# Optimization experiments

Hardware: AMD Instinct MI355X
Metric: run time of the kernel (lower is better)

## Reference

```python
import jax, jax.numpy as jnp
import numpy as np

TAU_MIN, TAU_MAX = 5.0, 50.0
BOOST = 3.2
DECO_RATE = 0.01

B, I, F, Q = 4096, 1024, 2048, 4

def setup_inputs() -> dict:
    key = jax.random.key(0)
    ks = jax.random.split(key, 12)
    return {
        "inputs": jax.random.normal(ks[0], (B, I), jnp.float32),
        "hidden_state": jax.random.normal(ks[1], (B, F), jnp.float32),
        "W_in": jax.random.normal(ks[2], (I, F), jnp.float32) / np.sqrt(I),
        "b_in": jnp.zeros((F,), jnp.float32),
        "amp_real": jax.random.normal(ks[3], (F, Q), jnp.float32) * 0.1,
        "amp_imag": jax.random.normal(ks[4], (F, Q), jnp.float32) * 0.1,
        "phase": jax.random.uniform(ks[5], (F, Q), jnp.float32, 0.0, 2 * np.pi),
        "primary": jax.random.normal(ks[6], (F, F), jnp.float32) / np.sqrt(F),
        "ent_mat": jax.random.normal(ks[7], (F, F), jnp.float32) / np.sqrt(F),
        "corr": jax.random.uniform(ks[8], (F,), jnp.float32, 0.0, 0.7),
        "W_tau": jax.random.uniform(ks[9], (F, F), jnp.float32, 0.0, 0.1) / np.sqrt(F),
        "b_tau": jnp.zeros((F,), jnp.float32),
        "W_dec": jax.random.uniform(ks[10], (F, F), jnp.float32, 0.0, 0.5) / np.sqrt(F),
        "b_dec": jnp.zeros((F,), jnp.float32),
        "time_step": 1,
    }

def reference(inputs, hidden_state, W_in, b_in, amp_real, amp_imag, phase,
              primary, ent_mat, corr, W_tau, b_tau, W_dec, b_dec, time_step):
    t = jnp.float32(time_step)
    batch = inputs.shape[0]
    feats = hidden_state.shape[1]

    # input projection: [B,I] @ [I,F]
    x_proj = inputs @ W_in + b_in

    # quantum superposition state (batch-independent, [F,Q] params)
    ph = phase + t * 0.1
    real_c = amp_real * jnp.cos(ph)          # [F,Q]
    imag_c = amp_imag * jnp.sin(ph)          # [F,Q]
    sup_r = real_c.sum(-1)                    # [F]
    sup_i = imag_c.sum(-1)                    # [F]
    prob_amp = real_c ** 2 + imag_c ** 2      # [F,Q]
    q_state = sup_r * jnp.exp(-sup_i ** 2)    # [F]
    q_state_b = jnp.broadcast_to(q_state, (batch, feats))
    prob_amp_b = jnp.broadcast_to(prob_amp, (batch,) + prob_amp.shape)

    # entangled recurrent connections: two F x F matmuls
    ent_rec = hidden_state @ primary + (hidden_state @ ent_mat) * corr

    # quantum time constants
    tau_raw = q_state_b @ W_tau + b_tau
    tau_q = (TAU_MIN + (TAU_MAX - TAU_MIN) * jax.nn.sigmoid(tau_raw)) / BOOST

    # decoherence gate
    deco = jax.nn.sigmoid(q_state_b @ W_dec + b_dec)
    coherent = jnp.exp(-DECO_RATE * t)

    classical = jnp.tanh(x_proj + ent_rec)
    quantum_act = q_state_b * deco * coherent
    combined = classical + quantum_act

    dx_dt = (-hidden_state + combined) / tau_q
    dt_q = 0.1 / BOOST
    new_hidden = hidden_state + dt_q * dx_dt

    # diagnostics
    d_amp = jnp.mean(prob_amp_b, axis=-1)          # [B,F]
    d_coh = coherent
    d_ent = jnp.mean(jnp.abs(ent_rec))
    d_dec = jnp.mean(deco)
    d_tau = jnp.mean(tau_q)
    return (new_hidden, d_amp, d_coh, d_ent, d_dec, d_tau)
```

## Files before the change

kernel.cpp:

```cpp
#include <hip/hip_runtime.h>
#include <hip/hip_bf16.h>

#define BD 4096
#define ID 1024
#define FD 2048

typedef __bf16 v8bf __attribute__((ext_vector_type(8)));
typedef float  v4f  __attribute__((ext_vector_type(4)));

struct alignas(8) bf4 { __hip_bfloat16 x, y, z, w; };

__device__ inline __hip_bfloat16 bf(float f) { return __float2bfloat16(f); }
__device__ inline float sig(float x) { return 1.f / (1.f + expf(-x)); }

__device__ inline void gload16(const __hip_bfloat16* g, __hip_bfloat16* l) {
  __builtin_amdgcn_global_load_lds(
      (const __attribute__((address_space(1))) void*)g,
      (__attribute__((address_space(3))) void*)l, 16, 0, 0);
}

__global__ void k_prep_q(const float* ar, const float* ai, const float* ph,
                         const int* tstep, float* qs, float* pamp,
                         float* scal, float* tau_raw, float* dec_raw) {
  int j = blockIdx.x * 256 + threadIdx.x;
  if (j < 4) scal[j] = 0.f;
  if (j < FD) { tau_raw[j] = 0.f; dec_raw[j] = 0.f; }
  if (j >= FD) return;
  float t = (float)tstep[0];
  float4 a = ((const float4*)ar)[j];
  float4 b = ((const float4*)ai)[j];
  float4 p = ((const float4*)ph)[j];
  float sr = 0.f, si = 0.f, pm = 0.f;
  {
    float c, s, rc, ic;
    c = cosf(p.x + 0.1f * t); s = sinf(p.x + 0.1f * t);
    rc = a.x * c; ic = b.x * s; sr += rc; si += ic; pm += rc * rc + ic * ic;
    c = cosf(p.y + 0.1f * t); s = sinf(p.y + 0.1f * t);
    rc = a.y * c; ic = b.y * s; sr += rc; si += ic; pm += rc * rc + ic * ic;
    c = cosf(p.z + 0.1f * t); s = sinf(p.z + 0.1f * t);
    rc = a.z * c; ic = b.z * s; sr += rc; si += ic; pm += rc * rc + ic * ic;
    c = cosf(p.w + 0.1f * t); s = sinf(p.w + 0.1f * t);
    rc = a.w * c; ic = b.w * s; sr += rc; si += ic; pm += rc * rc + ic * ic;
  }
  qs[j] = sr * expf(-si * si);
  pamp[j] = 0.25f * pm;
}

__global__ void k_cast(const float* s1, __hip_bfloat16* d1, int n1,
                       const float* s2, __hip_bfloat16* d2) {
  int i = blockIdx.x * blockDim.x + threadIdx.x;
  const float* src = s1; __hip_bfloat16* dst = d1;
  if (i >= n1) { i -= n1; src = s2; dst = d2; }
  float4 v = ((const float4*)src)[i];
  bf4 o{bf(v.x), bf(v.y), bf(v.z), bf(v.w)};
  ((bf4*)dst)[i] = o;
}

__global__ void k_tcast(const float* src, const float* src2, const float* corr,
                        __hip_bfloat16* dst, int R, int C, int useM) {
  __shared__ float t[32][33];
  int tx = threadIdx.x, ty = threadIdx.y;
  int x = blockIdx.x * 32 + tx;
  int yb = blockIdx.y * 32;
  float cr = useM ? corr[x] : 0.f;
#pragma unroll
  for (int j = 0; j < 4; j++) {
    int y = yb + ty + j * 8;
    float v = src[(size_t)y * C + x];
    if (useM) v += src2[(size_t)y * C + x] * cr;
    t[ty + j * 8][tx] = v;
  }
  __syncthreads();
#pragma unroll
  for (int j = 0; j < 4; j++) {
    int orow = blockIdx.x * 32 + ty + j * 8;
    int ocol = yb + tx;
    dst[(size_t)orow * R + ocol] = bf(t[tx][ty + j * 8]);
  }
}

__global__ void k_matvec(const float* qs, const float* Wt, const float* Wd,
                         float* tau_raw, float* dec_raw) {
  int j = blockIdx.x * 256 + threadIdx.x;
  int i0 = blockIdx.y * 128;
  const float* W = blockIdx.z ? Wd : Wt;
  float* out = blockIdx.z ? dec_raw : tau_raw;
  __shared__ float q[128];
  if (threadIdx.x < 128) q[threadIdx.x] = qs[i0 + threadIdx.x];
  __syncthreads();
  float acc = 0.f;
#pragma unroll 8
  for (int i = 0; i < 128; i++) acc = fmaf(q[i], W[(size_t)(i0 + i) * FD + j], acc);
  atomicAdd(&out[j], acc);
}

__global__ void k_post(const float* tau_raw, const float* dec_raw, const float* qs,
                       const float* b_tau, const float* b_dec, const int* tstep,
                       float* s_arr, float* qact, float* scal) {
  int j = blockIdx.x * 256 + threadIdx.x;
  float t = (float)tstep[0];
  float coh = expf(-0.01f * t);
  float tq = (5.f + 45.f * sig(tau_raw[j] + b_tau[j])) / 3.2f;
  s_arr[j] = 0.03125f / tq;
  float dec = sig(dec_raw[j] + b_dec[j]);
  qact[j] = qs[j] * dec * coh;
  float tsum = tq, dsum = dec;
  for (int off = 32; off; off >>= 1) {
    tsum += __shfl_down(tsum, off);
    dsum += __shfl_down(dsum, off);
  }
  __shared__ float rt[4], rd[4];
  int w = threadIdx.x >> 6;
  if ((threadIdx.x & 63) == 0) { rt[w] = tsum; rd[w] = dsum; }
  __syncthreads();
  if (threadIdx.x == 0) {
    atomicAdd(&scal[1], rd[0] + rd[1] + rd[2] + rd[3]);
    atomicAdd(&scal[2], rt[0] + rt[1] + rt[2] + rt[3]);
  }
}

__global__ __launch_bounds__(256, 4) void k_gemm(
    const __hip_bfloat16* __restrict__ Ah,
    const __hip_bfloat16* __restrict__ MT,
    const __hip_bfloat16* __restrict__ Ax,
    const __hip_bfloat16* __restrict__ WT,
    const float* __restrict__ b_in, const float* __restrict__ s_arr,
    const float* __restrict__ qact,
    float* ent_sum, float* __restrict__ out) {
  __shared__ alignas(16) __hip_bfloat16 As[2][128][32];
  __shared__ alignas(16) __hip_bfloat16 Bs[2][64][32];
  __shared__ float red[4];

  const int tid = threadIdx.x;
  const int l = tid & 63, w = tid >> 6;
  const int wr = w >> 1, wc = w & 1;
  const int row0 = blockIdx.x * 128, col0 = blockIdx.y * 64;

  v4f acc[4][2];
#pragma unroll
  for (int i = 0; i < 4; i++)
#pragma unroll
    for (int j = 0; j < 2; j++) acc[i][j] = (v4f)0.f;

  auto stage = [&](int buf, const __hip_bfloat16* A, int lda,
                   const __hip_bfloat16* B, int ldb, int k) {
    gload16(A + (size_t)(row0 + w * 32 + (l >> 2)) * lda + k + (l & 3) * 8,
            &As[buf][w * 32][0]);
    gload16(A + (size_t)(row0 + w * 32 + 16 + (l >> 2)) * lda + k + (l & 3) * 8,
            &As[buf][w * 32 + 16][0]);
    gload16(B + (size_t)(col0 + w * 16 + (l >> 2)) * ldb + k + (l & 3) * 8,
            &Bs[buf][w * 16][0]);
  };
  auto compute = [&](int buf) {
    v8bf a[4], b[2];
#pragma unroll
    for (int mi = 0; mi < 4; mi++)
      a[mi] = *(const v8bf*)&As[buf][wr * 64 + mi * 16 + (l & 15)][(l >> 4) * 8];
#pragma unroll
    for (int ni = 0; ni < 2; ni++)
      b[ni] = *(const v8bf*)&Bs[buf][wc * 32 + ni * 16 + (l & 15)][(l >> 4) * 8];
#pragma unroll
    for (int mi = 0; mi < 4; mi++)
#pragma unroll
      for (int ni = 0; ni < 2; ni++)
        acc[mi][ni] = __builtin_amdgcn_mfma_f32_16x16x32_bf16(a[mi], b[ni], acc[mi][ni], 0, 0, 0);
  };

  stage(0, Ah, FD, MT, FD, 0);
  __syncthreads();
  for (int kt = 0; kt < FD / 32; kt++) {
    if (kt + 1 < FD / 32) stage((kt + 1) & 1, Ah, FD, MT, FD, (kt + 1) * 32);
    compute(kt & 1);
    __syncthreads();
  }

  float asum = 0.f;
#pragma unroll
  for (int mi = 0; mi < 4; mi++)
#pragma unroll
    for (int ni = 0; ni < 2; ni++)
#pragma unroll
      for (int e = 0; e < 4; e++) asum += fabsf(acc[mi][ni][e]);

  stage(0, Ax, ID, WT, ID, 0);
  __syncthreads();
  for (int kt = 0; kt < ID / 32; kt++) {
    if (kt + 1 < ID / 32) stage((kt + 1) & 1, Ax, ID, WT, ID, (kt + 1) * 32);
    compute(kt & 1);
    __syncthreads();
  }

  for (int off = 32; off; off >>= 1) asum += __shfl_down(asum, off);
  if (l == 0) red[w] = asum;
  __syncthreads();
  if (tid == 0) atomicAdd(ent_sum, red[0] + red[1] + red[2] + red[3]);

#pragma unroll
  for (int ni = 0; ni < 2; ni++) {
    int gc = col0 + wc * 32 + ni * 16 + (l & 15);
    float bi = b_in[gc], qa = qact[gc], sj = s_arr[gc];
#pragma unroll
    for (int mi = 0; mi < 4; mi++) {
      int gr0 = row0 + wr * 64 + mi * 16 + (l >> 4) * 4;
#pragma unroll
      for (int e = 0; e < 4; e++) {
        int gr = gr0 + e;
        float comb = tanhf(acc[mi][ni][e] + bi) + qa;
        float h = __bfloat162float(Ah[(size_t)gr * FD + gc]);
        out[(size_t)gr * FD + gc] = fmaf(sj, comb - h, h);
      }
    }
  }
}

__global__ void k_damp(const float* __restrict__ pamp, const float* scal,
                       const int* tstep, float* __restrict__ out1, float* out3) {
  int i = blockIdx.x * 256 + threadIdx.x;
  int c = (i * 4) & (FD - 1);
  ((float4*)out1)[i] = *(const float4*)&pamp[c];
  if (i == 0) {
    float t = (float)tstep[0];
    out3[0] = expf(-0.01f * t);
    out3[1] = scal[0] / (float)((size_t)BD * FD);
    out3[2] = scal[1] / (float)FD;
    out3[3] = scal[2] / (float)FD;
  }
}

extern "C" void kernel_launch(void* const* d_in, const int* in_sizes, int n_in,
                              void* d_out, int out_size, void* d_ws, size_t ws_size,
                              hipStream_t stream) {
  const float* inputs  = (const float*)d_in[0];
  const float* hidden  = (const float*)d_in[1];
  const float* W_in    = (const float*)d_in[2];
  const float* b_in    = (const float*)d_in[3];
  const float* amp_r   = (const float*)d_in[4];
  const float* amp_i   = (const float*)d_in[5];
  const float* phase   = (const float*)d_in[6];
  const float* primary = (const float*)d_in[7];
  const float* ent_mat = (const float*)d_in[8];
  const float* corr    = (const float*)d_in[9];
  const float* W_tau   = (const float*)d_in[10];
  const float* b_tau   = (const float*)d_in[11];
  const float* W_dec   = (const float*)d_in[12];
  const float* b_dec   = (const float*)d_in[13];
  const int*   tstep   = (const int*)d_in[14];

  char* ws = (char*)d_ws;
  __hip_bfloat16* inputs_bf = (__hip_bfloat16*)(ws + 0);
  __hip_bfloat16* hidden_bf = (__hip_bfloat16*)(ws + 8388608);
  __hip_bfloat16* WT        = (__hip_bfloat16*)(ws + 25165824);
  __hip_bfloat16* MT        = (__hip_bfloat16*)(ws + 29360128);
  char* sb = ws + 37748736;
  float* scal    = (float*)(sb);
  float* qs      = (float*)(sb + 16);
  float* pamp    = (float*)(sb + 16 + 8192);
  float* tau_raw = (float*)(sb + 16 + 2 * 8192);
  float* dec_raw = (float*)(sb + 16 + 3 * 8192);
  float* s_arr   = (float*)(sb + 16 + 4 * 8192);
  float* qact    = (float*)(sb + 16 + 5 * 8192);

  float* out = (float*)d_out;

  hipLaunchKernelGGL(k_prep_q, dim3(8), dim3(256), 0, stream,
                     amp_r, amp_i, phase, tstep, qs, pamp, scal, tau_raw, dec_raw);
  hipLaunchKernelGGL(k_cast, dim3(12288), dim3(256), 0, stream,
                     inputs, inputs_bf, BD * ID / 4, hidden, hidden_bf);
  hipLaunchKernelGGL(k_tcast, dim3(64, 32), dim3(32, 8), 0, stream,
                     W_in, (const float*)nullptr, (const float*)nullptr, WT, ID, FD, 0);
  hipLaunchKernelGGL(k_tcast, dim3(64, 64), dim3(32, 8), 0, stream,
                     primary, ent_mat, corr, MT, FD, FD, 1);
  hipLaunchKernelGGL(k_matvec, dim3(8, 16, 2), dim3(256), 0, stream, qs, W_tau, W_dec, tau_raw, dec_raw);
  hipLaunchKernelGGL(k_post, dim3(8), dim3(256), 0, stream, tau_raw, dec_raw, qs, b_tau, b_dec, tstep, s_arr, qact, scal);
  hipLaunchKernelGGL(k_gemm, dim3(32, 32), dim3(256), 0, stream,
                     hidden_bf, MT, inputs_bf, WT, b_in, s_arr, qact,
                     &scal[0], out);
  hipLaunchKernelGGL(k_damp, dim3(8192), dim3(256), 0, stream,
                     pamp, scal, tstep, out + (size_t)BD * FD, out + (size_t)2 * BD * FD);
}
```

Measured before the change: 142.9 us.

## Switch GEMM operands to FP8 with scaled MFMA and XOR-swizzled LDS tiles

Converts activations and weights to FP8 instead of bf16 and uses the 16x16x128 scaled f8f6f4 MFMA with unit scales. The K tile grows to 128 and LDS reads use an XOR swizzle. This halves operand bytes and doubles matrix throughput per instruction. The epilogue now reads the fp32 hidden state directly instead of the quantized copy. FP8 (e4m3) greatly reduces GEMM precision, so accuracy against the reference is at risk.

```diff
diff --git a/kernel.cpp b/kernel.cpp
--- a/kernel.cpp
+++ b/kernel.cpp
@@ -1,19 +1,18 @@
 #include <hip/hip_runtime.h>
 #include <hip/hip_bf16.h>
+#include <stdint.h>
 
 #define BD 4096
 #define ID 1024
 #define FD 2048
 
-typedef __bf16 v8bf __attribute__((ext_vector_type(8)));
-typedef float  v4f  __attribute__((ext_vector_type(4)));
-
-struct alignas(8) bf4 { __hip_bfloat16 x, y, z, w; };
-
-__device__ inline __hip_bfloat16 bf(float f) { return __float2bfloat16(f); }
+typedef float v4f __attribute__((ext_vector_type(4)));
+typedef int   v4i __attribute__((ext_vector_type(4)));
+typedef int   v8i __attribute__((ext_vector_type(8)));
+
 __device__ inline float sig(float x) { return 1.f / (1.f + expf(-x)); }
 
-__device__ inline void gload16(const __hip_bfloat16* g, __hip_bfloat16* l) {
+__device__ inline void gload16(const uint8_t* g, uint8_t* l) {
   __builtin_amdgcn_global_load_lds(
       (const __attribute__((address_space(1))) void*)g,
       (__attribute__((address_space(3))) void*)l, 16, 0, 0);
@@ -46,18 +45,22 @@
   pamp[j] = 0.25f * pm;
 }
 
-__global__ void k_cast(const float* s1, __hip_bfloat16* d1, int n1,
-                       const float* s2, __hip_bfloat16* d2) {
+__global__ void k_cast8(const float* s1, uint8_t* d1, int n1,
+                        const float* s2, uint8_t* d2) {
   int i = blockIdx.x * blockDim.x + threadIdx.x;
-  const float* src = s1; __hip_bfloat16* dst = d1;
+  const float* src = s1; uint8_t* dst = d1;
   if (i >= n1) { i -= n1; src = s2; dst = d2; }
-  float4 v = ((const float4*)src)[i];
-  bf4 o{bf(v.x), bf(v.y), bf(v.z), bf(v.w)};
-  ((bf4*)dst)[i] = o;
-}
-
-__global__ void k_tcast(const float* src, const float* src2, const float* corr,
-                        __hip_bfloat16* dst, int R, int C, int useM) {
+  float4 v0 = ((const float4*)src)[i * 2];
+  float4 v1 = ((const float4*)src)[i * 2 + 1];
+  int p0 = __builtin_amdgcn_cvt_pk_fp8_f32(v0.x, v0.y, 0, 0);
+  p0 = __builtin_amdgcn_cvt_pk_fp8_f32(v0.z, v0.w, p0, 1);
+  int p1 = __builtin_amdgcn_cvt_pk_fp8_f32(v1.x, v1.y, 0, 0);
+  p1 = __builtin_amdgcn_cvt_pk_fp8_f32(v1.z, v1.w, p1, 1);
+  ((int2*)dst)[i] = make_int2(p0, p1);
+}
+
+__global__ void k_tcast8(const float* src, const float* src2, const float* corr,
+                         uint8_t* dst, int R, int C, int useM) {
   __shared__ float t[32][33];
   int tx = threadIdx.x, ty = threadIdx.y;
   int x = blockIdx.x * 32 + tx;
@@ -71,12 +74,14 @@
     t[ty + j * 8][tx] = v;
   }
   __syncthreads();
-#pragma unroll
-  for (int j = 0; j < 4; j++) {
-    int orow = blockIdx.x * 32 + ty + j * 8;
-    int ocol = yb + tx;
-    dst[(size_t)orow * R + ocol] = bf(t[tx][ty + j * 8]);
-  }
+  int tid = ty * 32 + tx;
+  int dr = tid >> 3;
+  int dc0 = (tid & 7) * 4;
+  float a0 = t[dc0 + 0][dr], a1 = t[dc0 + 1][dr];
+  float a2 = t[dc0 + 2][dr], a3 = t[dc0 + 3][dr];
+  int p = __builtin_amdgcn_cvt_pk_fp8_f32(a0, a1, 0, 0);
+  p = __builtin_amdgcn_cvt_pk_fp8_f32(a2, a3, p, 1);
+  *(int*)&dst[(size_t)(blockIdx.x * 32 + dr) * R + yb + dc0] = p;
 }
 
 __global__ void k_matvec(const float* qs, const float* Wt, const float* Wd,
@@ -119,16 +124,17 @@
   }
 }
 
-__global__ __launch_bounds__(256, 4) void k_gemm(
-    const __hip_bfloat16* __restrict__ Ah,
-    const __hip_bfloat16* __restrict__ MT,
-    const __hip_bfloat16* __restrict__ Ax,
-    const __hip_bfloat16* __restrict__ WT,
+__global__ __launch_bounds__(256) void k_gemm(
+    const uint8_t* __restrict__ Ah,
+    const uint8_t* __restrict__ MT,
+    const uint8_t* __restrict__ Ax,
+    const uint8_t* __restrict__ WT,
+    const float* __restrict__ hidden,
     const float* __restrict__ b_in, const float* __restrict__ s_arr,
     const float* __restrict__ qact,
     float* ent_sum, float* __restrict__ out) {
-  __shared__ alignas(16) __hip_bfloat16 As[2][128][32];
-  __shared__ alignas(16) __hip_bfloat16 Bs[2][64][32];
+  __shared__ alignas(16) uint8_t As[2][128][128];
+  __shared__ alignas(16) uint8_t Bs[2][64][128];
   __shared__ float red[4];
 
   const int tid = threadIdx.x;
@@ -142,34 +148,57 @@
 #pragma unroll
     for (int j = 0; j < 2; j++) acc[i][j] = (v4f)0.f;
 
-  auto stage = [&](int buf, const __hip_bfloat16* A, int lda,
-                   const __hip_bfloat16* B, int ldb, int k) {
-    gload16(A + (size_t)(row0 + w * 32 + (l >> 2)) * lda + k + (l & 3) * 8,
-            &As[buf][w * 32][0]);
-    gload16(A + (size_t)(row0 + w * 32 + 16 + (l >> 2)) * lda + k + (l & 3) * 8,
-            &As[buf][w * 32 + 16][0]);
-    gload16(B + (size_t)(col0 + w * 16 + (l >> 2)) * ldb + k + (l & 3) * 8,
-            &Bs[buf][w * 16][0]);
+  const int srow = l >> 3;
+  const int scol = ((l & 7) ^ srow) * 16;
+
+  auto stage = [&](int buf, const uint8_t* A, int lda,
+                   const uint8_t* B, int ldb, int k) {
+#pragma unroll
+    for (int i = 0; i < 4; i++)
+      gload16(A + (size_t)(row0 + w * 32 + i * 8 + srow) * lda + k + scol,
+              &As[buf][w * 32 + i * 8][0]);
+#pragma unroll
+    for (int i = 0; i < 2; i++)
+      gload16(B + (size_t)(col0 + w * 16 + i * 8 + srow) * ldb + k + scol,
+              &Bs[buf][w * 16 + i * 8][0]);
   };
+
   auto compute = [&](int buf) {
-    v8bf a[4], b[2];
+    const int s2 = (l >> 4) * 2, sw = l & 7;
+    v8i a[4], b[2];
+#pragma unroll
+    for (int mi = 0; mi < 4; mi++) {
+      int r = wr * 64 + mi * 16 + (l & 15);
+      v4i lo = *(const v4i*)&As[buf][r][((s2 + 0) ^ sw) * 16];
+      v4i hi = *(const v4i*)&As[buf][r][((s2 + 1) ^ sw) * 16];
+      v8i af;
+      af[0] = lo[0]; af[1] = lo[1]; af[2] = lo[2]; af[3] = lo[3];
+      af[4] = hi[0]; af[5] = hi[1]; af[6] = hi[2]; af[7] = hi[3];
+      a[mi] = af;
+    }
+#pragma unroll
+    for (int ni = 0; ni < 2; ni++) {
+      int r = wc * 32 + ni * 16 + (l & 15);
+      v4i lo = *(const v4i*)&Bs[buf][r][((s2 + 0) ^ sw) * 16];
+      v4i hi = *(const v4i*)&Bs[buf][r][((s2 + 1) ^ sw) * 16];
+      v8i bf8;
+      bf8[0] = lo[0]; bf8[1] = lo[1]; bf8[2] = lo[2]; bf8[3] = lo[3];
+      bf8[4] = hi[0]; bf8[5] = hi[1]; bf8[6] = hi[2]; bf8[7] = hi[3];
+      b[ni] = bf8;
+    }
 #pragma unroll
     for (int mi = 0; mi < 4; mi++)
-      a[mi] = *(const v8bf*)&As[buf][wr * 64 + mi * 16 + (l & 15)][(l >> 4) * 8];
-#pragma unroll
-    for (int ni = 0; ni < 2; ni++)
-      b[ni] = *(const v8bf*)&Bs[buf][wc * 32 + ni * 16 + (l & 15)][(l >> 4) * 8];
-#pragma unroll
-    for (int mi = 0; mi < 4; mi++)
 #pragma unroll
       for (int ni = 0; ni < 2; ni++)
-        acc[mi][ni] = __builtin_amdgcn_mfma_f32_16x16x32_bf16(a[mi], b[ni], acc[mi][ni], 0, 0, 0);
+        acc[mi][ni] = __builtin_amdgcn_mfma_scale_f32_16x16x128_f8f6f4(
+            a[mi], b[ni], acc[mi][ni], 0, 0,
+            0, 0x7F7F7F7F, 0, 0x7F7F7F7F);
   };
 
   stage(0, Ah, FD, MT, FD, 0);
   __syncthreads();
-  for (int kt = 0; kt < FD / 32; kt++) {
-    if (kt + 1 < FD / 32) stage((kt + 1) & 1, Ah, FD, MT, FD, (kt + 1) * 32);
+  for (int kt = 0; kt < 16; kt++) {
+    if (kt + 1 < 16) stage((kt + 1) & 1, Ah, FD, MT, FD, (kt + 1) * 128);
     compute(kt & 1);
     __syncthreads();
   }
@@ -184,8 +213,8 @@
 
   stage(0, Ax, ID, WT, ID, 0);
   __syncthreads();
-  for (int kt = 0; kt < ID / 32; kt++) {
-    if (kt + 1 < ID / 32) stage((kt + 1) & 1, Ax, ID, WT, ID, (kt + 1) * 32);
+  for (int kt = 0; kt < 8; kt++) {
+    if (kt + 1 < 8) stage((kt + 1) & 1, Ax, ID, WT, ID, (kt + 1) * 128);
     compute(kt & 1);
     __syncthreads();
   }
@@ -206,7 +235,7 @@
       for (int e = 0; e < 4; e++) {
         int gr = gr0 + e;
         float comb = tanhf(acc[mi][ni][e] + bi) + qa;
-        float h = __bfloat162float(Ah[(size_t)gr * FD + gc]);
+        float h = hidden[(size_t)gr * FD + gc];
         out[(size_t)gr * FD + gc] = fmaf(sj, comb - h, h);
       }
     }
@@ -247,11 +276,11 @@
   const int*   tstep   = (const int*)d_in[14];
 
   char* ws = (char*)d_ws;
-  __hip_bfloat16* inputs_bf = (__hip_bfloat16*)(ws + 0);
-  __hip_bfloat16* hidden_bf = (__hip_bfloat16*)(ws + 8388608);
-  __hip_bfloat16* WT        = (__hip_bfloat16*)(ws + 25165824);
-  __hip_bfloat16* MT        = (__hip_bfloat16*)(ws + 29360128);
-  char* sb = ws + 37748736;
+  uint8_t* inputs_f8 = (uint8_t*)(ws + 0);
+  uint8_t* hidden_f8 = (uint8_t*)(ws + 4194304);
+  uint8_t* WT        = (uint8_t*)(ws + 12582912);
+  uint8_t* MT        = (uint8_t*)(ws + 14680064);
+  char* sb = ws + 18874368;
   float* scal    = (float*)(sb);
   float* qs      = (float*)(sb + 16);
   float* pamp    = (float*)(sb + 16 + 8192);
@@ -264,16 +293,16 @@
 
   hipLaunchKernelGGL(k_prep_q, dim3(8), dim3(256), 0, stream,
                      amp_r, amp_i, phase, tstep, qs, pamp, scal, tau_raw, dec_raw);
-  hipLaunchKernelGGL(k_cast, dim3(12288), dim3(256), 0, stream,
-                     inputs, inputs_bf, BD * ID / 4, hidden, hidden_bf);
-  hipLaunchKernelGGL(k_tcast, dim3(64, 32), dim3(32, 8), 0, stream,
+  hipLaunchKernelGGL(k_cast8, dim3(6144), dim3(256), 0, stream,
+                     inputs, inputs_f8, BD * ID / 8, hidden, hidden_f8);
+  hipLaunchKernelGGL(k_tcast8, dim3(64, 32), dim3(32, 8), 0, stream,
                      W_in, (const float*)nullptr, (const float*)nullptr, WT, ID, FD, 0);
-  hipLaunchKernelGGL(k_tcast, dim3(64, 64), dim3(32, 8), 0, stream,
+  hipLaunchKernelGGL(k_tcast8, dim3(64, 64), dim3(32, 8), 0, stream,
                      primary, ent_mat, corr, MT, FD, FD, 1);
   hipLaunchKernelGGL(k_matvec, dim3(8, 16, 2), dim3(256), 0, stream, qs, W_tau, W_dec, tau_raw, dec_raw);
   hipLaunchKernelGGL(k_post, dim3(8), dim3(256), 0, stream, tau_raw, dec_raw, qs, b_tau, b_dec, tstep, s_arr, qact, scal);
   hipLaunchKernelGGL(k_gemm, dim3(32, 32), dim3(256), 0, stream,
-                     hidden_bf, MT, inputs_bf, WT, b_in, s_arr, qact,
+                     hidden_f8, MT, inputs_f8, WT, hidden, b_in, s_arr, qact,
                      &scal[0], out);
   hipLaunchKernelGGL(k_damp, dim3(8192), dim3(256), 0, stream,
                      pamp, scal, tstep, out + (size_t)BD * FD, out + (size_t)2 * BD * FD);
```

Measured after the change: 167.5 us. 17.2% more time.
